# Optimization experiments

Hardware: AMD Instinct MI355X
Metric: run time of the kernel (lower is better)

The kernel has to match this reference:

```python
import jax, jax.numpy as jnp
import numpy as np

N_NODES = 50000
N_EDGES = 1600000
D = 128
MU = 1.0
EPS = 1e-06


def setup_inputs() -> dict:
    key = jax.random.key(0)
    ks = jax.random.split(key, 6)
    x = jax.random.normal(ks[0], (N_NODES, D), dtype=jnp.float32)
    edge_index = jax.random.randint(ks[1], (2, N_EDGES), 0, N_NODES, dtype=jnp.int64)
    edge_weight = jax.random.uniform(ks[2], (N_EDGES,), dtype=jnp.float32)
    s = 1.0 / np.sqrt(D)  # nn.Linear-style init scale
    W_chi = jax.random.uniform(ks[3], (D, D), dtype=jnp.float32, minval=-s, maxval=s)
    W_phi = jax.random.uniform(ks[4], (D, D), dtype=jnp.float32, minval=-s, maxval=s)
    W_varphi = jax.random.uniform(ks[5], (D, D), dtype=jnp.float32, minval=-s, maxval=s)
    return {"x": x, "edge_index": edge_index, "edge_weight": edge_weight,
            "W_chi": W_chi, "W_phi": W_phi, "W_varphi": W_varphi}


def reference(x, edge_index, edge_weight, W_chi, W_phi, W_varphi):
    num_nodes = x.shape[0]
    row, col = edge_index[0], edge_index[1]

    # degree_i = sum of edge weights over outgoing edges (scatter_add by row)
    degree = jax.ops.segment_sum(edge_weight, row, num_segments=num_nodes)

    # Phi_chi: per-node tanh of L2 norm of Theta_chi(x)
    Phi_chi = jnp.tanh(jnp.linalg.norm(x @ W_chi.T, axis=1))  # [N]

    x_row = x[row]            # [E, D] gather
    x_col = x[col]            # [E, D] gather

    # Theta_phi(Theta_chi(.)) on gathered endpoints
    x_src = (x_row @ W_chi.T) @ W_phi.T   # [E, D]
    x_dst = (x_col @ W_chi.T) @ W_phi.T   # [E, D]
    Phi_phi = jnp.tanh(jnp.abs(jnp.sum(x_src * x_dst, axis=1)))  # [E]

    diff = x_row - x_col                  # [E, D]
    Phi_varphi = jnp.tanh(1.0 / (jnp.linalg.norm(diff @ W_varphi.T, axis=1) + EPS))  # [E]

    Phi = edge_weight / degree[row] * Phi_phi * Phi_varphi / Phi_chi[row]  # [E]

    energies = Phi[:, None] * diff        # [E, D]
    x_star = jax.ops.segment_sum(energies, row, num_segments=num_nodes)  # [N, D]

    return x - (1.0 / MU) * x_star
```

## Files before the change

### kernel.cpp

```cpp
#include <hip/hip_runtime.h>
#include <hip/hip_bf16.h>

#define NNODES 50000
#define NEDGES 1600000
#define DD 128
#define EPSF 1e-6f
#define NB_SCAN 196
#define NPART 64
#define EPP 25000
#define RGSZ 12500

using u32 = unsigned int;
using u16 = unsigned short;
using u64 = unsigned long long;
typedef __attribute__((ext_vector_type(8))) short v8s;
typedef __attribute__((ext_vector_type(4))) float v4f;
typedef __attribute__((ext_vector_type(4))) int   v4i;
typedef __attribute__((ext_vector_type(2))) float v2f;

static __device__ __forceinline__ float b2f16(u16 v) { return __uint_as_float(((u32)v) << 16); }
static __device__ __forceinline__ u16 f2b(float f) {
    u32 u = __float_as_uint(f);
    return (u16)((u + 0x7fffu + ((u >> 16) & 1u)) >> 16);
}
static __device__ __forceinline__ float tanh_pos(float a) {
    float e = __expf(-2.f * a);
    return __fdividef(1.f - e, 1.f + e);
}

#define OFF_GFRAG  0
#define OFF_PHICHI 98304
#define OFF_VSX    298304
#define OFF_CNT    698304
#define OFF_START  898304
#define OFF_BSUM   1098368
#define OFF_BOFF   1099392
#define OFF_ABSC   1100416
#define OFF_AQ     1500416
#define OFF_BQ     7900416
#define OFF_XB     14300416
#define OFF_XQ     27100416
#define OFF_EREC   33500416
#define OFF_WCOMB  33500416
#define OFF_RANK   39900416
#define OFF_CBASE  43100416
#define WS_NEED_RANK 55900416ull

static __device__ __forceinline__ void gstore(u16* gf, int mat, int a, int c, float v) {
    int lane = (((a >> 3) & 3) << 4) | (c & 15);
    int u = ((((mat*8 + (c >> 4))*4 + (a >> 5))*64 + lane) << 3) | (a & 7);
    gf[u] = f2b(v);
}

#define HB (NEDGES/256)
#define XBLK (NNODES/4)

__global__ __launch_bounds__(256) void k_hist(const int* __restrict__ ei,
                                              u16* __restrict__ rank,
                                              u32* __restrict__ cbase) {
    __shared__ u32 lcnt[RGSZ];
    int p = blockIdx.x >> 2, rg = blockIdx.x & 3;
    int t = threadIdx.x;
    for (int i = t; i < RGSZ; i += 256) lcnt[i] = 0;
    __syncthreads();
    int base = rg * RGSZ;
    for (int i = t; i < EPP; i += 256) {
        int e = p*EPP + i;
        int r = ei[e];
        u32 rr = (u32)(r - base);
        if (rr < RGSZ) {
            u32 old = atomicAdd(&lcnt[rr], 1u);
            rank[e] = (u16)old;
        }
    }
    __syncthreads();
    u32* dst = cbase + (size_t)p*NNODES + base;
    for (int i = t; i < RGSZ; i += 256) dst[i] = lcnt[i];
}

__global__ __launch_bounds__(256) void k_rowsum(u32* __restrict__ cbase,
                                                u32* __restrict__ cnt) {
    int r = blockIdx.x*256 + threadIdx.x;
    if (r >= NNODES) return;
    u32 running = 0;
    #pragma unroll
    for (int p = 0; p < NPART; ++p) {
        u32 c = cbase[(size_t)p*NNODES + r];
        cbase[(size_t)p*NNODES + r] = running;
        running += c;
    }
    cnt[r] = running;
}

template<bool RANK>
__global__ __launch_bounds__(256) void k_prep(const int* __restrict__ ei,
                                              const float* __restrict__ x,
                                              const float* __restrict__ Wchi,
                                              const float* __restrict__ Wphi,
                                              const float* __restrict__ Wvphi,
                                              u32* __restrict__ cnt,
                                              u16* __restrict__ xb,
                                              char* __restrict__ xq,
                                              float* __restrict__ vsx,
                                              float* __restrict__ wcomb,
                                              u16* __restrict__ gf) {
    int b = blockIdx.x, t = threadIdx.x;
    if (!RANK) {
        if (b < HB) {
            atomicAdd(&cnt[ei[b*256 + t]], 1u);
            return;
        }
        b -= HB;
    }
    if (b < XBLK) {
        int w = t >> 6, lane = t & 63;
        int node = b*4 + w;
        float2 xv = ((const float2*)(x + (size_t)node*DD))[lane];
        u32 pk = (u32)f2b(xv.x) | ((u32)f2b(xv.y) << 16);
        ((u32*)xb)[node*64 + lane] = pk;
        float m = fmaxf(fabsf(xv.x), fabsf(xv.y));
        #pragma unroll
        for (int mask = 1; mask < 64; mask <<= 1)
            m = fmaxf(m, __shfl_xor(m, mask));
        float inv = (m > 0.f) ? 127.f/m : 0.f;
        int q0 = (int)rintf(xv.x*inv), q1 = (int)rintf(xv.y*inv);
        ((u16*)xq)[node*64 + lane] = (u16)((q0 & 0xff) | ((q1 & 0xff) << 8));
        if (lane == 0) vsx[2*node + 1] = m * (1.f/127.f);
        return;
    }
    int bb = b - XBLK;
    if (bb < 64) {
        int idx = bb*256 + t;
        int i = idx >> 7, k = idx & 127;
        float acc = 0.f;
        #pragma unroll 8
        for (int m = 0; m < DD; ++m)
            acc = fmaf(Wphi[i*DD+m], Wchi[m*DD+k], acc);
        wcomb[i*DD+k] = acc;
    } else {
        const float* W = (bb < 128) ? Wvphi : Wchi;
        int mat = (bb < 128) ? 1 : 2;
        int idx = ((bb & 63))*256 + t;
        int a = idx >> 7, c = idx & 127;
        float acc = 0.f;
        #pragma unroll 8
        for (int m = 0; m < DD; ++m)
            acc = fmaf(W[m*DD+a], W[m*DD+c], acc);
        gstore(gf, mat, a, c, acc);
    }
}

__global__ __launch_bounds__(256) void k_scan_bsum(const u32* __restrict__ cnt,
                                                   u32* __restrict__ bsum,
                                                   const float* __restrict__ wcomb,
                                                   u16* __restrict__ gf) {
    if (blockIdx.x >= NB_SCAN) {
        int idx = (blockIdx.x - NB_SCAN)*256 + threadIdx.x;
        int a = idx >> 7, c = idx & 127;
        float acc = 0.f;
        #pragma unroll 8
        for (int m = 0; m < DD; ++m)
            acc = fmaf(wcomb[m*DD+a], wcomb[m*DD+c], acc);
        gstore(gf, 0, a, c, acc);
        return;
    }
    __shared__ u32 s[256];
    int i = blockIdx.x*256 + threadIdx.x;
    s[threadIdx.x] = (i < NNODES) ? cnt[i] : 0u;
    __syncthreads();
    for (int off = 128; off > 0; off >>= 1) {
        if (threadIdx.x < off) s[threadIdx.x] += s[threadIdx.x + off];
        __syncthreads();
    }
    if (threadIdx.x == 0) bsum[blockIdx.x] = s[0];
}

__global__ __launch_bounds__(256) void k_scan_boff(const u32* __restrict__ bsum,
                                                   u32* __restrict__ boff) {
    __shared__ u32 s[256];
    int t = threadIdx.x;
    u32 v = (t < NB_SCAN) ? bsum[t] : 0u;
    s[t] = v;
    __syncthreads();
    for (int off = 1; off < 256; off <<= 1) {
        u32 a = (t >= off) ? s[t - off] : 0u;
        __syncthreads();
        s[t] += a;
        __syncthreads();
    }
    if (t < NB_SCAN) boff[t] = s[t] - v;
}

__global__ __launch_bounds__(256) void k_scan_final(const u32* __restrict__ cnt,
                                                    const u32* __restrict__ boff,
                                                    u32* __restrict__ start,
                                                    u32* __restrict__ cursor) {
    __shared__ u32 s[256];
    int t = threadIdx.x;
    int i = blockIdx.x*256 + t;
    u32 v = (i < NNODES) ? cnt[i] : 0u;
    s[t] = v;
    __syncthreads();
    for (int off = 1; off < 256; off <<= 1) {
        u32 a = (t >= off) ? s[t - off] : 0u;
        __syncthreads();
        s[t] += a;
        __syncthreads();
    }
    if (i < NNODES) {
        u32 val = boff[blockIdx.x] + (s[t] - v);
        start[i]  = val;
        cursor[i] = val;
        if (i == NNODES-1) start[NNODES] = val + v;
    }
}

#define SB (NEDGES/256)
#define GB 782

template<bool RANK>
__global__ __launch_bounds__(256) void k_mid(const int* __restrict__ ei,
                                             const float* __restrict__ ew,
                                             const u32* __restrict__ start,
                                             u32* __restrict__ cursor,
                                             const u16* __restrict__ rank,
                                             const u32* __restrict__ cbase,
                                             u32* __restrict__ erec,
                                             const u16* __restrict__ xb,
                                             float* __restrict__ ws,
                                             char* __restrict__ aq,
                                             char* __restrict__ bq,
                                             float* __restrict__ absc) {
    int b = blockIdx.x, t = threadIdx.x;
    if (b % 9 != 0) {
        int eb = b - b/9 - 1;
        int e = eb*256 + t;
        int r = __builtin_nontemporal_load(&ei[e]);
        u32 pos;
        if (RANK) {
            int p = e / EPP;
            pos = start[r] + cbase[(size_t)p*NNODES + r]
                + (u32)__builtin_nontemporal_load(&rank[e]);
        } else {
            pos = atomicAdd(&cursor[r], 1u);
        }
        u32 c  = (u32)__builtin_nontemporal_load(&ei[NEDGES + e]);
        u32 wb = (u32)f2b(__builtin_nontemporal_load(&ew[e])) & 0x7fffu;
        erec[pos] = (c << 15) | wb;
        return;
    }
    __shared__ u16 xs[4][16][DD];
    int w = t >> 6, l = t & 63;
    int l15 = l & 15, lq = l >> 4;
    int nb = (b/9)*64 + w*16;
    if (nb >= NNODES) return;

    const v8s* xbv = (const v8s*)(xb + (size_t)(nb + l15)*DD);
    v8s af[4];
    #pragma unroll
    for (int kk = 0; kk < 4; ++kk) {
        af[kk] = xbv[kk*4 + lq];
        *(v8s*)&xs[w][l15][kk*32 + lq*8] = af[kk];
    }
    const v8s* gf = (const v8s*)ws;
    float* phichi = ws + OFF_PHICHI/4;
    float* vsx    = ws + OFF_VSX/4;
    float sa4[4] = {0.f, 0.f, 0.f, 0.f};

    #pragma unroll
    for (int mat = 0; mat < 3; ++mat) {
        v4f acc[8];
        #pragma unroll
        for (int nt = 0; nt < 8; ++nt) acc[nt] = (v4f){0.f,0.f,0.f,0.f};
        #pragma unroll
        for (int kk = 0; kk < 4; ++kk)
            #pragma unroll
            for (int nt = 0; nt < 8; ++nt)
                acc[nt] = __builtin_amdgcn_mfma_f32_16x16x32_bf16(
                    af[kk], gf[((mat*8 + nt)*4 + kk)*64 + l], acc[nt], 0, 0, 0);
        if (mat < 2) {
            float mx[4] = {0.f, 0.f, 0.f, 0.f};
            #pragma unroll
            for (int nt = 0; nt < 8; ++nt)
                #pragma unroll
                for (int r = 0; r < 4; ++r)
                    mx[r] = fmaxf(mx[r], fabsf(acc[nt][r]));
            #pragma unroll
            for (int mask = 1; mask < 16; mask <<= 1)
                #pragma unroll
                for (int r = 0; r < 4; ++r)
                    mx[r] = fmaxf(mx[r], __shfl_xor(mx[r], mask));
            float iv[4], sc[4];
            #pragma unroll
            for (int r = 0; r < 4; ++r) {
                iv[r] = (mx[r] > 0.f) ? 127.f/mx[r] : 0.f;
                sc[r] = mx[r] * (1.f/127.f);
            }
            char* qdst = mat ? bq : aq;
            #pragma unroll
            for (int nt = 0; nt < 8; ++nt)
                #pragma unroll
                for (int r = 0; r < 4; ++r)
                    qdst[(size_t)(nb + lq*4 + r)*128 + nt*16 + l15] =
                        (char)(int)rintf(acc[nt][r]*iv[r]);
            if (mat == 0) {
                #pragma unroll
                for (int r = 0; r < 4; ++r) sa4[r] = sc[r];
            } else if (l15 == 0) {
                #pragma unroll
                for (int r = 0; r < 4; ++r)
                    *(v2f*)&absc[2*(nb + lq*4 + r)] = (v2f){sa4[r], sc[r]};
            }
        }
        if (mat >= 1) {
            float p0 = 0.f, p1 = 0.f, p2 = 0.f, p3 = 0.f;
            #pragma unroll
            for (int nt = 0; nt < 8; ++nt) {
                int nn = nt*16 + l15;
                p0 = fmaf(b2f16(xs[w][lq*4+0][nn]), acc[nt][0], p0);
                p1 = fmaf(b2f16(xs[w][lq*4+1][nn]), acc[nt][1], p1);
                p2 = fmaf(b2f16(xs[w][lq*4+2][nn]), acc[nt][2], p2);
                p3 = fmaf(b2f16(xs[w][lq*4+3][nn]), acc[nt][3], p3);
            }
            #pragma unroll
            for (int mask = 1; mask < 16; mask <<= 1) {
                p0 += __shfl_xor(p0, mask);
                p1 += __shfl_xor(p1, mask);
                p2 += __shfl_xor(p2, mask);
                p3 += __shfl_xor(p3, mask);
            }
            if (l15 == 0) {
                int n0 = nb + lq*4;
                if (mat == 1) {
                    vsx[2*(n0+0)] = p0; vsx[2*(n0+1)] = p1;
                    vsx[2*(n0+2)] = p2; vsx[2*(n0+3)] = p3;
                } else {
                    phichi[n0+0] = tanh_pos(sqrtf(fmaxf(p0, 0.f)));
                    phichi[n0+1] = tanh_pos(sqrtf(fmaxf(p1, 0.f)));
                    phichi[n0+2] = tanh_pos(sqrtf(fmaxf(p2, 0.f)));
                    phichi[n0+3] = tanh_pos(sqrtf(fmaxf(p3, 0.f)));
                }
            }
        }
    }
}

__global__ __launch_bounds__(256) void k_accum(const float* __restrict__ x,
                                               const float* __restrict__ phichi,
                                               const float* __restrict__ vsx,
                                               const float* __restrict__ absc,
                                               const u32* __restrict__ start,
                                               const u32* __restrict__ erec,
                                               const char* __restrict__ xq,
                                               const char* __restrict__ aq,
                                               const char* __restrict__ bq,
                                               float* __restrict__ out) {
    __shared__ float red[4][8][132];
    int w = threadIdx.x >> 6, lane = threadIdx.x & 63;
    int node = blockIdx.x*4 + w;
    int l15 = lane & 15, lq = lane >> 4;

    u32 s0 = start[node];
    u32 n  = start[node+1] - s0;
    float vq_r = vsx[2*node];
    float2 sab = *(const float2*)&absc[2*node];

    v4i zero4 = {0, 0, 0, 0};
    v4i afr[2];
    {
        const char* src = (l15 == 1) ? bq : aq;
        const v4i* p = (const v4i*)(src + (size_t)node*128);
        bool keep = (l15 < 2);
        #pragma unroll
        for (int kk = 0; kk < 2; ++kk) {
            v4i v = p[kk*4 + lq];
            afr[kk] = keep ? v : zero4;
        }
    }

    float accl[2][16];
    #pragma unroll
    for (int kk = 0; kk < 2; ++kk)
        #pragma unroll
        for (int j = 0; j < 16; ++j) accl[kk][j] = 0.f;
    float sphi = 0.f, wsum = 0.f;

    u32 ntiles = (n + 15) >> 4;

    auto ldr = [&](u32 tt) -> u32 {
        u32 off = tt*16 + (u32)l15;
        u32 eidx = (off < n) ? (s0 + off) : s0;
        return __builtin_nontemporal_load(&erec[eidx]);
    };

    if (ntiles) {
        u32 rc = ldr(0);
        u32 rn = (ntiles > 1) ? ldr(1) : rc;
        v4i pb0, pb1; float2 pvx;
        {
            u32 c0 = rc >> 15;
            const v4i* xcv = (const v4i*)(xq + (size_t)c0*128);
            pb0 = xcv[lq]; pb1 = xcv[4 + lq];
            pvx = *(const float2*)&vsx[2*c0];
        }
        for (u32 tt = 0; tt < ntiles; ++tt) {
            v4i b0 = pb0, b1 = pb1;
            float2 vx = pvx;
            u32 cur = rc;
            u32 rnn = (tt + 2 < ntiles) ? ldr(tt + 2) : rn;
            if (tt + 1 < ntiles) {
                u32 c1 = rn >> 15;
                const v4i* xcv = (const v4i*)(xq + (size_t)c1*128);
                pb0 = xcv[lq]; pb1 = xcv[4 + lq];
                pvx = *(const float2*)&vsx[2*c1];
            }
            rc = rn; rn = rnn;

            bool valid = (tt*16 + (u32)l15) < n;
            float w_e = valid ? __uint_as_float((cur & 0x7fffu) << 16) : 0.f;

            v4i d = zero4;
            d = __builtin_amdgcn_mfma_i32_16x16x64_i8(afr[0], b0, d, 0, 0, 0);
            d = __builtin_amdgcn_mfma_i32_16x16x64_i8(afr[1], b1, d, 0, 0, 0);
            float adot = (float)d[0] * (sab.x * vx.y);
            float bdot = (float)d[1] * (sab.y * vx.y);
            float ss = fmaxf(vq_r + vx.x - 2.f*bdot, 0.f);
            float psi = w_e * tanh_pos(fabsf(adot)) * tanh_pos(__fdividef(1.f, sqrtf(ss) + EPSF));
            float psi_b = __shfl(psi, l15);
            sphi += psi_b;
            wsum += w_e;
            float psx = psi_b * vx.y;
            #pragma unroll
            for (int kk = 0; kk < 2; ++kk) {
                const int* pw = (const int*)((kk == 0) ? &b0 : &b1);
                #pragma unroll
                for (int wd = 0; wd < 4; ++wd) {
                    int word = pw[wd];
                    accl[kk][wd*4+0] = fmaf(psx, (float)((word << 24) >> 24), accl[kk][wd*4+0]);
                    accl[kk][wd*4+1] = fmaf(psx, (float)((word << 16) >> 24), accl[kk][wd*4+1]);
                    accl[kk][wd*4+2] = fmaf(psx, (float)((word <<  8) >> 24), accl[kk][wd*4+2]);
                    accl[kk][wd*4+3] = fmaf(psx, (float)( word        >> 24), accl[kk][wd*4+3]);
                }
            }
        }
    }

    #pragma unroll
    for (int mask = 1; mask < 16; mask <<= 1) {
        sphi += __shfl_xor(sphi, mask);
        wsum += __shfl_xor(wsum, mask);
    }

    #pragma unroll
    for (int kk = 0; kk < 2; ++kk)
        #pragma unroll
        for (int j = 0; j < 16; ++j)
            accl[kk][j] += __shfl_xor(accl[kk][j], 1);

    if ((l15 & 1) == 0) {
        int e8 = l15 >> 1;
        #pragma unroll
        for (int kk = 0; kk < 2; ++kk) {
            int base = kk*64 + lq*16;
            *(float4*)&red[w][e8][base]      = *(float4*)&accl[kk][0];
            *(float4*)&red[w][e8][base + 4]  = *(float4*)&accl[kk][4];
            *(float4*)&red[w][e8][base + 8]  = *(float4*)&accl[kk][8];
            *(float4*)&red[w][e8][base + 12] = *(float4*)&accl[kk][12];
        }
    }
    __syncthreads();
    float a0 = 0.f, a1 = 0.f;
    #pragma unroll
    for (int e = 0; e < 8; ++e) {
        float2 v = *(const float2*)&red[w][e][lane*2];
        a0 += v.x; a1 += v.y;
    }

    float ia = (n == 0) ? 0.f : __fdividef(1.f, wsum * phichi[node]);
    float scale = 1.f - ia * sphi;
    float2 xv = *(const float2*)(x + (size_t)node*DD + lane*2);
    v2f o;
    o.x = xv.x*scale + ia*a0;
    o.y = xv.y*scale + ia*a1;
    __builtin_nontemporal_store(o, (v2f*)(out + (size_t)node*DD + lane*2));
}

extern "C" void kernel_launch(void* const* d_in, const int* in_sizes, int n_in,
                              void* d_out, int out_size, void* d_ws, size_t ws_size,
                              hipStream_t stream) {
    const float* x     = (const float*)d_in[0];
    const int*   ei    = (const int*)d_in[1];
    const float* ew    = (const float*)d_in[2];
    const float* Wchi  = (const float*)d_in[3];
    const float* Wphi  = (const float*)d_in[4];
    const float* Wvphi = (const float*)d_in[5];
    float* out = (float*)d_out;
    float* ws  = (float*)d_ws;
    char*  wsb = (char*)d_ws;

    float* phichi = (float*)(wsb + OFF_PHICHI);
    float* vsx    = (float*)(wsb + OFF_VSX);
    u32*   cnt    = (u32*)  (wsb + OFF_CNT);
    u32*   cursor = (u32*)  (wsb + OFF_CNT);
    u32*   start  = (u32*)  (wsb + OFF_START);
    u32*   bsum   = (u32*)  (wsb + OFF_BSUM);
    u32*   boff   = (u32*)  (wsb + OFF_BOFF);
    u16*   gf     = (u16*)  (wsb + OFF_GFRAG);
    float* absc   = (float*)(wsb + OFF_ABSC);
    char*  aq     = (char*) (wsb + OFF_AQ);
    char*  bq     = (char*) (wsb + OFF_BQ);
    u16*   xb     = (u16*)  (wsb + OFF_XB);
    char*  xq     = (char*) (wsb + OFF_XQ);
    u32*   erec   = (u32*)  (wsb + OFF_EREC);
    float* wcomb  = (float*)(wsb + OFF_WCOMB);
    u16*   rank   = (u16*)  (wsb + OFF_RANK);
    u32*   cbase  = (u32*)  (wsb + OFF_CBASE);

    bool use_rank = (ws_size >= (size_t)WS_NEED_RANK);

    if (use_rank) {
        k_hist<<<dim3(256), dim3(256), 0, stream>>>(ei, rank, cbase);
        k_prep<true><<<dim3(XBLK+192), dim3(256), 0, stream>>>(ei, x, Wchi, Wphi, Wvphi,
                                                               cnt, xb, xq, vsx, wcomb, gf);
        k_rowsum<<<dim3(NB_SCAN), dim3(256), 0, stream>>>(cbase, cnt);
    } else {
        hipError_t err = hipMemsetAsync(wsb + OFF_CNT, 0, 200000, stream);
        (void)err;
        k_prep<false><<<dim3(HB+XBLK+192), dim3(256), 0, stream>>>(ei, x, Wchi, Wphi, Wvphi,
                                                                   cnt, xb, xq, vsx, wcomb, gf);
    }
    k_scan_bsum<<<dim3(NB_SCAN+64), dim3(256), 0, stream>>>(cnt, bsum, wcomb, gf);
    k_scan_boff<<<dim3(1), dim3(256), 0, stream>>>(bsum, boff);
    k_scan_final<<<dim3(NB_SCAN), dim3(256), 0, stream>>>(cnt, boff, start, cursor);
    if (use_rank) {
        k_mid<true><<<dim3(SB+GB), dim3(256), 0, stream>>>(ei, ew, start, cursor, rank, cbase,
                                                           erec, xb, ws, aq, bq, absc);
    } else {
        k_mid<false><<<dim3(SB+GB), dim3(256), 0, stream>>>(ei, ew, start, cursor, rank, cbase,
                                                            erec, xb, ws, aq, bq, absc);
    }
    k_accum<<<dim3(NNODES/4), dim3(256), 0, stream>>>(x, phichi, vsx, absc, start, erec,
                                                      xq, aq, bq, out);
}
```

Baseline: 219.6 us.

## Fuse rowsum into block-sum kernel, deepen gather prefetch, cheaper int8 unpack

```diff
diff --git a/kernel.cpp b/kernel.cpp
--- a/kernel.cpp
+++ b/kernel.cpp
@@ -76,20 +76,6 @@
     __syncthreads();
     u32* dst = cbase + (size_t)p*NNODES + base;
     for (int i = t; i < RGSZ; i += 256) dst[i] = lcnt[i];
-}
-
-__global__ __launch_bounds__(256) void k_rowsum(u32* __restrict__ cbase,
-                                                u32* __restrict__ cnt) {
-    int r = blockIdx.x*256 + threadIdx.x;
-    if (r >= NNODES) return;
-    u32 running = 0;
-    #pragma unroll
-    for (int p = 0; p < NPART; ++p) {
-        u32 c = cbase[(size_t)p*NNODES + r];
-        cbase[(size_t)p*NNODES + r] = running;
-        running += c;
-    }
-    cnt[r] = running;
 }
 
 template<bool RANK>
@@ -150,10 +136,12 @@
     }
 }
 
-__global__ __launch_bounds__(256) void k_scan_bsum(const u32* __restrict__ cnt,
-                                                   u32* __restrict__ bsum,
-                                                   const float* __restrict__ wcomb,
-                                                   u16* __restrict__ gf) {
+template<bool RANK>
+__global__ __launch_bounds__(256) void k_rowsum_bsum(u32* __restrict__ cbase,
+                                                     u32* __restrict__ cnt,
+                                                     u32* __restrict__ bsum,
+                                                     const float* __restrict__ wcomb,
+                                                     u16* __restrict__ gf) {
     if (blockIdx.x >= NB_SCAN) {
         int idx = (blockIdx.x - NB_SCAN)*256 + threadIdx.x;
         int a = idx >> 7, c = idx & 127;
@@ -165,8 +153,22 @@
         return;
     }
     __shared__ u32 s[256];
-    int i = blockIdx.x*256 + threadIdx.x;
-    s[threadIdx.x] = (i < NNODES) ? cnt[i] : 0u;
+    int r = blockIdx.x*256 + threadIdx.x;
+    u32 running = 0;
+    if (RANK) {
+        if (r < NNODES) {
+            #pragma unroll
+            for (int p = 0; p < NPART; ++p) {
+                u32 c = cbase[(size_t)p*NNODES + r];
+                cbase[(size_t)p*NNODES + r] = running;
+                running += c;
+            }
+            cnt[r] = running;
+        }
+    } else {
+        running = (r < NNODES) ? cnt[r] : 0u;
+    }
+    s[threadIdx.x] = (r < NNODES) ? running : 0u;
     __syncthreads();
     for (int off = 128; off > 0; off >>= 1) {
         if (threadIdx.x < off) s[threadIdx.x] += s[threadIdx.x + off];
@@ -383,7 +385,7 @@
     for (int kk = 0; kk < 2; ++kk)
         #pragma unroll
         for (int j = 0; j < 16; ++j) accl[kk][j] = 0.f;
-    float sphi = 0.f, wsum = 0.f;
+    float sphi = 0.f, wsum = 0.f, Ctot = 0.f;
 
     u32 ntiles = (n + 15) >> 4;
 
@@ -396,25 +398,34 @@
     if (ntiles) {
         u32 rc = ldr(0);
         u32 rn = (ntiles > 1) ? ldr(1) : rc;
-        v4i pb0, pb1; float2 pvx;
+        u32 rm = (ntiles > 2) ? ldr(2) : rn;
+        v4i d0a, d0b; float2 d0v;
+        v4i d1a, d1b; float2 d1v;
         {
-            u32 c0 = rc >> 15;
-            const v4i* xcv = (const v4i*)(xq + (size_t)c0*128);
-            pb0 = xcv[lq]; pb1 = xcv[4 + lq];
-            pvx = *(const float2*)&vsx[2*c0];
+            u32 c = rc >> 15;
+            const v4i* p = (const v4i*)(xq + (size_t)c*128);
+            d0a = p[lq]; d0b = p[4 + lq];
+            d0v = *(const float2*)&vsx[2*c];
+        }
+        {
+            u32 c = rn >> 15;
+            const v4i* p = (const v4i*)(xq + (size_t)c*128);
+            d1a = p[lq]; d1b = p[4 + lq];
+            d1v = *(const float2*)&vsx[2*c];
         }
         for (u32 tt = 0; tt < ntiles; ++tt) {
-            v4i b0 = pb0, b1 = pb1;
-            float2 vx = pvx;
+            v4i b0 = d0a, b1 = d0b;
+            float2 vx = d0v;
             u32 cur = rc;
-            u32 rnn = (tt + 2 < ntiles) ? ldr(tt + 2) : rn;
-            if (tt + 1 < ntiles) {
-                u32 c1 = rn >> 15;
-                const v4i* xcv = (const v4i*)(xq + (size_t)c1*128);
-                pb0 = xcv[lq]; pb1 = xcv[4 + lq];
-                pvx = *(const float2*)&vsx[2*c1];
-            }
-            rc = rn; rn = rnn;
+            d0a = d1a; d0b = d1b; d0v = d1v;
+            if (tt + 2 < ntiles) {
+                u32 c = rm >> 15;
+                const v4i* p = (const v4i*)(xq + (size_t)c*128);
+                d1a = p[lq]; d1b = p[4 + lq];
+                d1v = *(const float2*)&vsx[2*c];
+            }
+            rc = rn; rn = rm;
+            rm = (tt + 3 < ntiles) ? ldr(tt + 3) : rm;
 
             bool valid = (tt*16 + (u32)l15) < n;
             float w_e = valid ? __uint_as_float((cur & 0x7fffu) << 16) : 0.f;
@@ -430,19 +441,29 @@
             sphi += psi_b;
             wsum += w_e;
             float psx = psi_b * vx.y;
+            Ctot += psx;
             #pragma unroll
             for (int kk = 0; kk < 2; ++kk) {
-                const int* pw = (const int*)((kk == 0) ? &b0 : &b1);
+                const v4i* bp = (kk == 0) ? &b0 : &b1;
                 #pragma unroll
                 for (int wd = 0; wd < 4; ++wd) {
-                    int word = pw[wd];
-                    accl[kk][wd*4+0] = fmaf(psx, (float)((word << 24) >> 24), accl[kk][wd*4+0]);
-                    accl[kk][wd*4+1] = fmaf(psx, (float)((word << 16) >> 24), accl[kk][wd*4+1]);
-                    accl[kk][wd*4+2] = fmaf(psx, (float)((word <<  8) >> 24), accl[kk][wd*4+2]);
-                    accl[kk][wd*4+3] = fmaf(psx, (float)( word        >> 24), accl[kk][wd*4+3]);
+                    u32 wx = ((u32)(*bp)[wd]) ^ 0x80808080u;
+                    accl[kk][wd*4+0] = fmaf(psx, (float)( wx        & 0xFFu), accl[kk][wd*4+0]);
+                    accl[kk][wd*4+1] = fmaf(psx, (float)((wx >>  8) & 0xFFu), accl[kk][wd*4+1]);
+                    accl[kk][wd*4+2] = fmaf(psx, (float)((wx >> 16) & 0xFFu), accl[kk][wd*4+2]);
+                    accl[kk][wd*4+3] = fmaf(psx, (float)( wx >> 24        ), accl[kk][wd*4+3]);
                 }
             }
         }
+    }
+
+    {
+        float corr = Ctot * 128.f;
+        #pragma unroll
+        for (int kk = 0; kk < 2; ++kk)
+            #pragma unroll
+            for (int j = 0; j < 16; ++j)
+                accl[kk][j] -= corr;
     }
 
     #pragma unroll
@@ -522,14 +543,16 @@
         k_hist<<<dim3(256), dim3(256), 0, stream>>>(ei, rank, cbase);
         k_prep<true><<<dim3(XBLK+192), dim3(256), 0, stream>>>(ei, x, Wchi, Wphi, Wvphi,
                                                                cnt, xb, xq, vsx, wcomb, gf);
-        k_rowsum<<<dim3(NB_SCAN), dim3(256), 0, stream>>>(cbase, cnt);
+        k_rowsum_bsum<true><<<dim3(NB_SCAN+64), dim3(256), 0, stream>>>(cbase, cnt, bsum,
+                                                                        wcomb, gf);
     } else {
         hipError_t err = hipMemsetAsync(wsb + OFF_CNT, 0, 200000, stream);
         (void)err;
         k_prep<false><<<dim3(HB+XBLK+192), dim3(256), 0, stream>>>(ei, x, Wchi, Wphi, Wvphi,
                                                                    cnt, xb, xq, vsx, wcomb, gf);
-    }
-    k_scan_bsum<<<dim3(NB_SCAN+64), dim3(256), 0, stream>>>(cnt, bsum, wcomb, gf);
+        k_rowsum_bsum<false><<<dim3(NB_SCAN+64), dim3(256), 0, stream>>>(cbase, cnt, bsum,
+                                                                         wcomb, gf);
+    }
     k_scan_boff<<<dim3(1), dim3(256), 0, stream>>>(bsum, boff);
     k_scan_final<<<dim3(NB_SCAN), dim3(256), 0, stream>>>(cnt, boff, start, cursor);
     if (use_rank) {
```

New measurement: 220.0 us. Within noise of the previous version (+0.2%).

## Fuse row-sum into block-sum scan, fold offset scan, restructure accum prefetch

Applied to the files above, without the earlier changes.

```diff
diff --git a/kernel.cpp b/kernel.cpp
--- a/kernel.cpp
+++ b/kernel.cpp
@@ -34,7 +34,6 @@
 #define OFF_CNT    698304
 #define OFF_START  898304
 #define OFF_BSUM   1098368
-#define OFF_BOFF   1099392
 #define OFF_ABSC   1100416
 #define OFF_AQ     1500416
 #define OFF_BQ     7900416
@@ -76,20 +75,6 @@
     __syncthreads();
     u32* dst = cbase + (size_t)p*NNODES + base;
     for (int i = t; i < RGSZ; i += 256) dst[i] = lcnt[i];
-}
-
-__global__ __launch_bounds__(256) void k_rowsum(u32* __restrict__ cbase,
-                                                u32* __restrict__ cnt) {
-    int r = blockIdx.x*256 + threadIdx.x;
-    if (r >= NNODES) return;
-    u32 running = 0;
-    #pragma unroll
-    for (int p = 0; p < NPART; ++p) {
-        u32 c = cbase[(size_t)p*NNODES + r];
-        cbase[(size_t)p*NNODES + r] = running;
-        running += c;
-    }
-    cnt[r] = running;
 }
 
 template<bool RANK>
@@ -150,10 +135,12 @@
     }
 }
 
-__global__ __launch_bounds__(256) void k_scan_bsum(const u32* __restrict__ cnt,
-                                                   u32* __restrict__ bsum,
-                                                   const float* __restrict__ wcomb,
-                                                   u16* __restrict__ gf) {
+template<bool RANK>
+__global__ __launch_bounds__(256) void k_rowsum_bsum(u32* __restrict__ cbase,
+                                                     u32* __restrict__ cnt,
+                                                     u32* __restrict__ bsum,
+                                                     const float* __restrict__ wcomb,
+                                                     u16* __restrict__ gf) {
     if (blockIdx.x >= NB_SCAN) {
         int idx = (blockIdx.x - NB_SCAN)*256 + threadIdx.x;
         int a = idx >> 7, c = idx & 127;
@@ -165,8 +152,22 @@
         return;
     }
     __shared__ u32 s[256];
-    int i = blockIdx.x*256 + threadIdx.x;
-    s[threadIdx.x] = (i < NNODES) ? cnt[i] : 0u;
+    int r = blockIdx.x*256 + threadIdx.x;
+    u32 running = 0;
+    if (RANK) {
+        if (r < NNODES) {
+            #pragma unroll
+            for (int p = 0; p < NPART; ++p) {
+                u32 c = cbase[(size_t)p*NNODES + r];
+                cbase[(size_t)p*NNODES + r] = running;
+                running += c;
+            }
+            cnt[r] = running;
+        }
+    } else {
+        running = (r < NNODES) ? cnt[r] : 0u;
+    }
+    s[threadIdx.x] = (r < NNODES) ? running : 0u;
     __syncthreads();
     for (int off = 128; off > 0; off >>= 1) {
         if (threadIdx.x < off) s[threadIdx.x] += s[threadIdx.x + off];
@@ -175,28 +176,22 @@
     if (threadIdx.x == 0) bsum[blockIdx.x] = s[0];
 }
 
-__global__ __launch_bounds__(256) void k_scan_boff(const u32* __restrict__ bsum,
-                                                   u32* __restrict__ boff) {
-    __shared__ u32 s[256];
-    int t = threadIdx.x;
-    u32 v = (t < NB_SCAN) ? bsum[t] : 0u;
-    s[t] = v;
-    __syncthreads();
-    for (int off = 1; off < 256; off <<= 1) {
-        u32 a = (t >= off) ? s[t - off] : 0u;
-        __syncthreads();
-        s[t] += a;
-        __syncthreads();
-    }
-    if (t < NB_SCAN) boff[t] = s[t] - v;
-}
-
 __global__ __launch_bounds__(256) void k_scan_final(const u32* __restrict__ cnt,
-                                                    const u32* __restrict__ boff,
+                                                    const u32* __restrict__ bsum,
                                                     u32* __restrict__ start,
                                                     u32* __restrict__ cursor) {
     __shared__ u32 s[256];
+    __shared__ u32 sb[256];
     int t = threadIdx.x;
+    u32 pre = 0;
+    for (int j = t; j < (int)blockIdx.x; j += 256) pre += bsum[j];
+    sb[t] = pre;
+    __syncthreads();
+    for (int off = 128; off > 0; off >>= 1) {
+        if (t < off) sb[t] += sb[t + off];
+        __syncthreads();
+    }
+    u32 boff = sb[0];
     int i = blockIdx.x*256 + t;
     u32 v = (i < NNODES) ? cnt[i] : 0u;
     s[t] = v;
@@ -208,7 +203,7 @@
         __syncthreads();
     }
     if (i < NNODES) {
-        u32 val = boff[blockIdx.x] + (s[t] - v);
+        u32 val = boff + (s[t] - v);
         start[i]  = val;
         cursor[i] = val;
         if (i == NNODES-1) start[NNODES] = val + v;
@@ -371,11 +366,9 @@
         const char* src = (l15 == 1) ? bq : aq;
         const v4i* p = (const v4i*)(src + (size_t)node*128);
         bool keep = (l15 < 2);
-        #pragma unroll
-        for (int kk = 0; kk < 2; ++kk) {
-            v4i v = p[kk*4 + lq];
-            afr[kk] = keep ? v : zero4;
-        }
+        v4i v0 = p[lq], v1 = p[4 + lq];
+        afr[0] = keep ? v0 : zero4;
+        afr[1] = keep ? v1 : zero4;
     }
 
     float accl[2][16];
@@ -393,55 +386,58 @@
         return __builtin_nontemporal_load(&erec[eidx]);
     };
 
+    auto body = [&](u32 tt, u32 cur, v4i b0, v4i b1, float2 vx) {
+        bool valid = (tt*16 + (u32)l15) < n;
+        float w_e = valid ? __uint_as_float((cur & 0x7fffu) << 16) : 0.f;
+        v4i d = zero4;
+        d = __builtin_amdgcn_mfma_i32_16x16x64_i8(afr[0], b0, d, 0, 0, 0);
+        d = __builtin_amdgcn_mfma_i32_16x16x64_i8(afr[1], b1, d, 0, 0, 0);
+        float adot = (float)d[0] * (sab.x * vx.y);
+        float bdot = (float)d[1] * (sab.y * vx.y);
+        float ss = fmaxf(vq_r + vx.x - 2.f*bdot, 0.f);
+        float psi = w_e * tanh_pos(fabsf(adot)) * tanh_pos(__fdividef(1.f, sqrtf(ss) + EPSF));
+        float psi_b = __shfl(psi, l15);
+        sphi += psi_b;
+        wsum += w_e;
+        float psx = psi_b * vx.y;
+        #pragma unroll
+        for (int kk = 0; kk < 2; ++kk) {
+            const int* pw = (const int*)((kk == 0) ? &b0 : &b1);
+            #pragma unroll
+            for (int wd = 0; wd < 4; ++wd) {
+                int word = pw[wd];
+                accl[kk][wd*4+0] = fmaf(psx, (float)((word << 24) >> 24), accl[kk][wd*4+0]);
+                accl[kk][wd*4+1] = fmaf(psx, (float)((word << 16) >> 24), accl[kk][wd*4+1]);
+                accl[kk][wd*4+2] = fmaf(psx, (float)((word <<  8) >> 24), accl[kk][wd*4+2]);
+                accl[kk][wd*4+3] = fmaf(psx, (float)( word        >> 24), accl[kk][wd*4+3]);
+            }
+        }
+    };
+
     if (ntiles) {
-        u32 rc = ldr(0);
-        u32 rn = (ntiles > 1) ? ldr(1) : rc;
-        v4i pb0, pb1; float2 pvx;
-        {
-            u32 c0 = rc >> 15;
-            const v4i* xcv = (const v4i*)(xq + (size_t)c0*128);
-            pb0 = xcv[lq]; pb1 = xcv[4 + lq];
-            pvx = *(const float2*)&vsx[2*c0];
-        }
-        for (u32 tt = 0; tt < ntiles; ++tt) {
-            v4i b0 = pb0, b1 = pb1;
-            float2 vx = pvx;
-            u32 cur = rc;
-            u32 rnn = (tt + 2 < ntiles) ? ldr(tt + 2) : rn;
-            if (tt + 1 < ntiles) {
-                u32 c1 = rn >> 15;
-                const v4i* xcv = (const v4i*)(xq + (size_t)c1*128);
-                pb0 = xcv[lq]; pb1 = xcv[4 + lq];
-                pvx = *(const float2*)&vsx[2*c1];
-            }
-            rc = rn; rn = rnn;
-
-            bool valid = (tt*16 + (u32)l15) < n;
-            float w_e = valid ? __uint_as_float((cur & 0x7fffu) << 16) : 0.f;
-
-            v4i d = zero4;
-            d = __builtin_amdgcn_mfma_i32_16x16x64_i8(afr[0], b0, d, 0, 0, 0);
-            d = __builtin_amdgcn_mfma_i32_16x16x64_i8(afr[1], b1, d, 0, 0, 0);
-            float adot = (float)d[0] * (sab.x * vx.y);
-            float bdot = (float)d[1] * (sab.y * vx.y);
-            float ss = fmaxf(vq_r + vx.x - 2.f*bdot, 0.f);
-            float psi = w_e * tanh_pos(fabsf(adot)) * tanh_pos(__fdividef(1.f, sqrtf(ss) + EPSF));
-            float psi_b = __shfl(psi, l15);
-            sphi += psi_b;
-            wsum += w_e;
-            float psx = psi_b * vx.y;
-            #pragma unroll
-            for (int kk = 0; kk < 2; ++kk) {
-                const int* pw = (const int*)((kk == 0) ? &b0 : &b1);
-                #pragma unroll
-                for (int wd = 0; wd < 4; ++wd) {
-                    int word = pw[wd];
-                    accl[kk][wd*4+0] = fmaf(psx, (float)((word << 24) >> 24), accl[kk][wd*4+0]);
-                    accl[kk][wd*4+1] = fmaf(psx, (float)((word << 16) >> 24), accl[kk][wd*4+1]);
-                    accl[kk][wd*4+2] = fmaf(psx, (float)((word <<  8) >> 24), accl[kk][wd*4+2]);
-                    accl[kk][wd*4+3] = fmaf(psx, (float)( word        >> 24), accl[kk][wd*4+3]);
-                }
-            }
+        u32 np = (ntiles < 4u) ? ntiles : 4u;
+        u32 rr[4]; v4i ba[4], bb[4]; float2 vv[4];
+        #pragma unroll
+        for (int i = 0; i < 4; ++i)
+            if ((u32)i < np) rr[i] = ldr((u32)i);
+        #pragma unroll
+        for (int i = 0; i < 4; ++i)
+            if ((u32)i < np) {
+                u32 c = rr[i] >> 15;
+                const v4i* p = (const v4i*)(xq + (size_t)c*128);
+                ba[i] = p[lq]; bb[i] = p[4 + lq];
+                vv[i] = *(const float2*)&vsx[2*c];
+            }
+        #pragma unroll
+        for (int i = 0; i < 4; ++i)
+            if ((u32)i < np) body((u32)i, rr[i], ba[i], bb[i], vv[i]);
+        for (u32 tt = 4; tt < ntiles; ++tt) {
+            u32 rc = ldr(tt);
+            u32 c = rc >> 15;
+            const v4i* p = (const v4i*)(xq + (size_t)c*128);
+            v4i b0 = p[lq], b1 = p[4 + lq];
+            float2 vx = *(const float2*)&vsx[2*c];
+            body(tt, rc, b0, b1, vx);
         }
     }
 
@@ -468,7 +464,6 @@
             *(float4*)&red[w][e8][base + 12] = *(float4*)&accl[kk][12];
         }
     }
-    __syncthreads();
     float a0 = 0.f, a1 = 0.f;
     #pragma unroll
     for (int e = 0; e < 8; ++e) {
@@ -504,7 +499,6 @@
     u32*   cursor = (u32*)  (wsb + OFF_CNT);
     u32*   start  = (u32*)  (wsb + OFF_START);
     u32*   bsum   = (u32*)  (wsb + OFF_BSUM);
-    u32*   boff   = (u32*)  (wsb + OFF_BOFF);
     u16*   gf     = (u16*)  (wsb + OFF_GFRAG);
     float* absc   = (float*)(wsb + OFF_ABSC);
     char*  aq     = (char*) (wsb + OFF_AQ);
@@ -522,16 +516,17 @@
         k_hist<<<dim3(256), dim3(256), 0, stream>>>(ei, rank, cbase);
         k_prep<true><<<dim3(XBLK+192), dim3(256), 0, stream>>>(ei, x, Wchi, Wphi, Wvphi,
                                                                cnt, xb, xq, vsx, wcomb, gf);
-        k_rowsum<<<dim3(NB_SCAN), dim3(256), 0, stream>>>(cbase, cnt);
+        k_rowsum_bsum<true><<<dim3(NB_SCAN+64), dim3(256), 0, stream>>>(cbase, cnt, bsum,
+                                                                        wcomb, gf);
     } else {
         hipError_t err = hipMemsetAsync(wsb + OFF_CNT, 0, 200000, stream);
         (void)err;
         k_prep<false><<<dim3(HB+XBLK+192), dim3(256), 0, stream>>>(ei, x, Wchi, Wphi, Wvphi,
                                                                    cnt, xb, xq, vsx, wcomb, gf);
-    }
-    k_scan_bsum<<<dim3(NB_SCAN+64), dim3(256), 0, stream>>>(cnt, bsum, wcomb, gf);
-    k_scan_boff<<<dim3(1), dim3(256), 0, stream>>>(bsum, boff);
-    k_scan_final<<<dim3(NB_SCAN), dim3(256), 0, stream>>>(cnt, boff, start, cursor);
+        k_rowsum_bsum<false><<<dim3(NB_SCAN+64), dim3(256), 0, stream>>>(cbase, cnt, bsum,
+                                                                         wcomb, gf);
+    }
+    k_scan_final<<<dim3(NB_SCAN), dim3(256), 0, stream>>>(cnt, bsum, start, cursor);
     if (use_rank) {
         k_mid<true><<<dim3(SB+GB), dim3(256), 0, stream>>>(ei, ew, start, cursor, rank, cbase,
                                                            erec, xb, ws, aq, bq, absc);
```

Measured after the change: 227.0 us. 1.03x slower.
